# Kernel tuning notes

Measured on AMD Instinct MI355X. Metric: run time of the kernel, lower is better.

## Reference

```python
import jax, jax.numpy as jnp
import numpy as np

P = 512        # number of graph pairs
MAXN = 192     # max(len_s) by construction
D_IN = 32      # num_input_features
HID = 64       # hidden_dim
REG = 0.1      # entropic reg
ITERS = 8      # numItermax in forward call
DEG = 8        # avg degree for synthetic edges


def setup_inputs() -> dict:
    key = jax.random.key(0)
    ks = jax.random.split(key, 16)
    len_s = np.asarray(96 + (np.arange(P) % 97), dtype=np.int32)          # 96..192
    len_t = np.asarray(32 + ((np.arange(P) * 7) % 65), dtype=np.int32)    # 32..96 <= len_s
    Ns, Nt = int(len_s.sum()), int(len_t.sum())
    return {
        "x_s": jax.random.normal(ks[0], (Ns, D_IN), jnp.float32),
        "x_t": jax.random.normal(ks[1], (Nt, D_IN), jnp.float32),
        "W_rel0": 0.1 * jax.random.normal(ks[2], (D_IN, HID), jnp.float32),
        "b_rel0": 0.1 * jax.random.normal(ks[3], (HID,), jnp.float32),
        "W_root0": 0.1 * jax.random.normal(ks[4], (D_IN, HID), jnp.float32),
        "W_rel1": 0.1 * jax.random.normal(ks[5], (HID, HID), jnp.float32),
        "b_rel1": 0.1 * jax.random.normal(ks[6], (HID,), jnp.float32),
        "W_root1": 0.1 * jax.random.normal(ks[7], (HID, HID), jnp.float32),
        "W_e": 0.1 * jax.random.normal(ks[8], (D_IN + 2 * HID, 64), jnp.float32),
        "b_e": 0.1 * jax.random.normal(ks[9], (64,), jnp.float32),
        "virtual": jax.random.uniform(ks[10], (64,), jnp.float32),
        "edge_index_s": jax.random.randint(ks[11], (2, Ns * DEG), 0, Ns, dtype=jnp.int32),
        "edge_index_t": jax.random.randint(ks[12], (2, Nt * DEG), 0, Nt, dtype=jnp.int32),
        "len_s": jnp.asarray(len_s),
        "len_t": jnp.asarray(len_t),
    }


def _normalize(x):
    return x / jnp.clip(jnp.linalg.norm(x, axis=-1, keepdims=True), 1e-12)


def _gnn_embed(x, ei, layers, W_e, b_e):
    # GraphConv: out = lin_rel(sum_{j->i} x_j) + lin_root(x_i), then relu; cat all layer outputs
    outs = [x]
    h = x
    for (Wr, br, Wo) in layers:
        agg = jax.ops.segment_sum(h[ei[0]], ei[1], num_segments=h.shape[0])
        h = jax.nn.relu(agg @ Wr + br + h @ Wo)
        outs.append(h)
    emb = jnp.concatenate(outs, axis=1) @ W_e + b_e
    return _normalize(emb)


def _pad_gather(emb, lens):
    # [total, E] -> [P, MAXN, E] via per-pair offsets (indices clipped; invalid masked later)
    off = jnp.cumsum(lens) - lens
    idx = jnp.clip(off[:, None] + jnp.arange(MAXN)[None, :], 0, emb.shape[0] - 1)
    return emb[idx]


def reference(x_s, x_t, W_rel0, b_rel0, W_root0, W_rel1, b_rel1, W_root1,
              W_e, b_e, virtual, edge_index_s, edge_index_t, len_s, len_t):
    layers = [(W_rel0, b_rel0, W_root0), (W_rel1, b_rel1, W_root1)]
    emb_s = _gnn_embed(x_s, edge_index_s, layers, W_e, b_e)  # [Ns, 64]
    emb_t = _gnn_embed(x_t, edge_index_t, layers, W_e, b_e)  # [Nt, 64]
    virt = _normalize(virtual[None, :])[0]

    s_pad = _pad_gather(emb_s, len_s)  # [P, MAXN, 64]
    t_pad = _pad_gather(emb_t, len_t)  # [P, MAXN, 64]
    j = jnp.arange(MAXN)
    # columns >= len_t use the virtual node embedding (covers j in [m, n))
    t_mask = (j[None, :] < len_t[:, None])[:, :, None]
    t_aug = jnp.where(t_mask, t_pad, virt[None, None, :])

    # Euclidean cdist via quadratic expansion
    sq_s = jnp.sum(s_pad * s_pad, -1)                              # [P, MAXN]
    sq_t = jnp.sum(t_aug * t_aug, -1)                              # [P, MAXN]
    dot = jnp.einsum('pid,pjd->pij', s_pad, t_aug)                 # [P, MAXN, MAXN]
    cd = jnp.sqrt(jnp.maximum(sq_s[:, :, None] + sq_t[:, None, :] - 2.0 * dot, 1e-12))

    # padded cost: real block = cdist, bottom-right pad block = 0, rest = 1000
    row_valid = j[None, :] < len_s[:, None]                        # [P, MAXN] (n = len_s)
    in_block = row_valid[:, :, None] & row_valid[:, None, :]
    pad_block = (~row_valid)[:, :, None] & (~row_valid)[:, None, :]
    cost = jnp.where(in_block, cd, jnp.where(pad_block, 0.0, 1000.0))

    # Sinkhorn-Knopp, a = b = ones(MAXN) so Kp = K and updates are 1/(K v), 1/(K^T u)
    K = jnp.exp(-cost / REG)

    def body(_, uv):
        u, v = uv
        v = 1.0 / jnp.einsum('pij,pi->pj', K, u)
        u = 1.0 / jnp.einsum('pij,pj->pi', K, v)
        return (u, v)

    u0 = jnp.full((P, MAXN), 1.0 / MAXN, dtype=cost.dtype)
    u, v = jax.lax.fori_loop(0, ITERS, body, (u0, u0))
    gamma = jax.lax.stop_gradient(u[:, :, None] * K * v[:, None, :])

    geds = jnp.sum(gamma * cost, axis=(1, 2))
    geds2 = geds / (len_s + len_t).astype(cost.dtype)
    return gamma, cost, geds2
```

## Files before the change

### kernel.cpp

```cpp
#include <hip/hip_runtime.h>
#include <math.h>

#define PAIRS 512
#define MAXN 192

__global__ void offsets_kernel(const int* __restrict__ ls, const int* __restrict__ lt,
                               int* __restrict__ off) {
    __shared__ int wa[8], wb[8];
    int t = threadIdx.x;
    int a = ls[t], b = lt[t];
    int ia = a, ib = b;
#pragma unroll
    for (int d = 1; d < 64; d <<= 1) {
        int xa = __shfl_up(ia, d, 64);
        int xb = __shfl_up(ib, d, 64);
        if ((t & 63) >= d) { ia += xa; ib += xb; }
    }
    if ((t & 63) == 63) { wa[t >> 6] = ia; wb[t >> 6] = ib; }
    __syncthreads();
    int pa = 0, pb = 0;
    for (int w = 0; w < (t >> 6); w++) { pa += wa[w]; pb += wb[w]; }
    off[t] = pa + ia - a;
    off[PAIRS + t] = pb + ib - b;
}

__global__ __launch_bounds__(256) void count2_kernel(const int* __restrict__ eiS,
                                                     const int* __restrict__ eiT,
                                                     int* __restrict__ cnt,
                                                     int Es, int Et, int split) {
    int e = blockIdx.x * 256 + threadIdx.x;
    if (e < Es) atomicAdd(&cnt[eiS[Es + e]], 1);
    else if (e < Es + Et) atomicAdd(&cnt[split + eiT[Et + (e - Es)]], 1);
}

__global__ __launch_bounds__(256) void scan1_kernel(int* __restrict__ data,
                                                    int* __restrict__ blockSums, int N) {
    __shared__ int sc[256];
    int t = threadIdx.x;
    int base = blockIdx.x * 1024;
    int v[4];
    int s = 0;
#pragma unroll
    for (int q = 0; q < 4; q++) {
        int i = base + t * 4 + q;
        v[q] = (i < N) ? data[i] : 0;
        s += v[q];
    }
    sc[t] = s;
    __syncthreads();
    for (int d = 1; d < 256; d <<= 1) {
        int x = (t >= d) ? sc[t - d] : 0;
        __syncthreads();
        sc[t] += x;
        __syncthreads();
    }
    int excl = sc[t] - s;
#pragma unroll
    for (int q = 0; q < 4; q++) {
        int i = base + t * 4 + q;
        if (i < N) { data[i] = excl; excl += v[q]; }
    }
    if (t == 255) blockSums[blockIdx.x] = sc[255];
}

__global__ void scan2_kernel(int* __restrict__ blockSums, int B) {
    __shared__ int sh[256];
    int t = threadIdx.x;
    int v = (t < B) ? blockSums[t] : 0;
    sh[t] = v;
    __syncthreads();
    for (int d = 1; d < 256; d <<= 1) {
        int x = (t >= d) ? sh[t - d] : 0;
        __syncthreads();
        sh[t] += x;
        __syncthreads();
    }
    if (t < B) blockSums[t] = sh[t] - v;
}

__global__ __launch_bounds__(256) void scan3_kernel(int* __restrict__ data,
                                                    const int* __restrict__ blockSums,
                                                    int* __restrict__ cursor, int N) {
    int i = blockIdx.x * 256 + threadIdx.x;
    if (i < N) {
        int v = data[i] + blockSums[i >> 10];
        data[i] = v;
        cursor[i] = v;
    }
}

__global__ __launch_bounds__(256) void fill2_kernel(const int* __restrict__ eiS,
                                                    const int* __restrict__ eiT,
                                                    int* __restrict__ cursor,
                                                    int* __restrict__ src,
                                                    int Es, int Et, int split) {
    int e = blockIdx.x * 256 + threadIdx.x;
    if (e < Es) {
        int p = atomicAdd(&cursor[eiS[Es + e]], 1);
        src[p] = eiS[e];
    } else if (e < Es + Et) {
        int ee = e - Es;
        int p = atomicAdd(&cursor[split + eiT[Et + ee]], 1);
        src[p] = eiT[ee];
    }
}

template <int F>
__global__ __launch_bounds__(256) void gather_kernel(const float* __restrict__ featA,
                                                     const float* __restrict__ featB,
                                                     int split,
                                                     const int* __restrict__ rs,
                                                     const int* __restrict__ re,
                                                     const int* __restrict__ src,
                                                     float* __restrict__ agg, int N) {
    int gid = blockIdx.x * 256 + threadIdx.x;
    int row = gid / F;
    int lane = threadIdx.x & (F - 1);
    if (row >= N) return;
    int b = rs[row], e = re[row];
    int cnt = e - b;
    const float* feat = (row < split) ? featA : featB;
    int pre = cnt < F ? cnt : F;
    int sidx = (lane < cnt) ? src[b + lane] : 0;
    float acc = 0.f;
    for (int q = 0; q < pre; q++) {
        int s = __shfl(sidx, q, F);
        acc += feat[(size_t)s * F + lane];
    }
    for (int q = b + F; q < e; q++) acc += feat[(size_t)src[q] * F + lane];
    agg[(size_t)row * F + lane] = acc;
}

template <int KIN>
__global__ __launch_bounds__(256) void lin_gemm_kernel(const float* __restrict__ agg,
    const float* __restrict__ hinA, const float* __restrict__ hinB, int split,
    const float* __restrict__ Wrel, const float* __restrict__ brel,
    const float* __restrict__ Wroot, float* __restrict__ hout, int N) {
    __shared__ float Abuf[64 * 65];
    __shared__ float4 Wbuf[64 * 16];
    int tid = threadIdx.x;
    int i = tid & 15, j = tid >> 4;
    int rowbase = blockIdx.x * 64;
    float4 bv = ((const float4*)brel)[j];
    float acc[4][4];
#pragma unroll
    for (int r = 0; r < 4; r++) { acc[r][0] = bv.x; acc[r][1] = bv.y; acc[r][2] = bv.z; acc[r][3] = bv.w; }

    for (int c0 = 0; c0 < 2 * KIN; c0 += 64) {
        __syncthreads();
        for (int t = tid; t < 1024; t += 256) {
            int r = t >> 4, k4 = t & 15;
            int kg = c0 + 4 * k4;
            int row = rowbase + r; if (row >= N) row = N - 1;
            float4 v;
            if (kg < KIN) {
                v = ((const float4*)(agg + (size_t)row * KIN))[kg >> 2];
            } else {
                int kk = kg - KIN;
                const float* h = (row < split) ? hinA + (size_t)row * KIN
                                               : hinB + (size_t)(row - split) * KIN;
                v = ((const float4*)h)[kk >> 2];
            }
            float* d = Abuf + r * 65 + 4 * k4;
            d[0] = v.x; d[1] = v.y; d[2] = v.z; d[3] = v.w;
        }
        for (int t = tid; t < 1024; t += 256) {
            int k = t >> 4, jj = t & 15;
            int kg = c0 + k;
            const float* Wsrc = (kg < KIN) ? (Wrel + (size_t)kg * 64)
                                           : (Wroot + (size_t)(kg - KIN) * 64);
            Wbuf[t] = ((const float4*)Wsrc)[jj];
        }
        __syncthreads();
#pragma unroll 4
        for (int k = 0; k < 64; k++) {
            float4 wv = Wbuf[k * 16 + j];
            float a0 = Abuf[(4 * i + 0) * 65 + k];
            float a1 = Abuf[(4 * i + 1) * 65 + k];
            float a2 = Abuf[(4 * i + 2) * 65 + k];
            float a3 = Abuf[(4 * i + 3) * 65 + k];
            acc[0][0] = fmaf(a0, wv.x, acc[0][0]); acc[0][1] = fmaf(a0, wv.y, acc[0][1]);
            acc[0][2] = fmaf(a0, wv.z, acc[0][2]); acc[0][3] = fmaf(a0, wv.w, acc[0][3]);
            acc[1][0] = fmaf(a1, wv.x, acc[1][0]); acc[1][1] = fmaf(a1, wv.y, acc[1][1]);
            acc[1][2] = fmaf(a1, wv.z, acc[1][2]); acc[1][3] = fmaf(a1, wv.w, acc[1][3]);
            acc[2][0] = fmaf(a2, wv.x, acc[2][0]); acc[2][1] = fmaf(a2, wv.y, acc[2][1]);
            acc[2][2] = fmaf(a2, wv.z, acc[2][2]); acc[2][3] = fmaf(a2, wv.w, acc[2][3]);
            acc[3][0] = fmaf(a3, wv.x, acc[3][0]); acc[3][1] = fmaf(a3, wv.y, acc[3][1]);
            acc[3][2] = fmaf(a3, wv.z, acc[3][2]); acc[3][3] = fmaf(a3, wv.w, acc[3][3]);
        }
    }
#pragma unroll
    for (int r = 0; r < 4; r++) {
        int row = rowbase + 4 * i + r;
        if (row < N) {
            float4 o = make_float4(fmaxf(acc[r][0], 0.f), fmaxf(acc[r][1], 0.f),
                                   fmaxf(acc[r][2], 0.f), fmaxf(acc[r][3], 0.f));
            ((float4*)(hout + (size_t)row * 64))[j] = o;
        }
    }
}

__global__ __launch_bounds__(256) void emb_gemm_kernel(const float* __restrict__ xA,
    const float* __restrict__ xB, int split,
    const float* __restrict__ h1, const float* __restrict__ h2,
    const float* __restrict__ We, const float* __restrict__ be,
    float* __restrict__ emb, int N) {
    __shared__ float Abuf[64 * 65];
    __shared__ float4 Wbuf[64 * 16];
    int tid = threadIdx.x;
    int i = tid & 15, j = tid >> 4;
    int rowbase = blockIdx.x * 64;
    float4 bv = ((const float4*)be)[j];
    float acc[4][4];
#pragma unroll
    for (int r = 0; r < 4; r++) { acc[r][0] = bv.x; acc[r][1] = bv.y; acc[r][2] = bv.z; acc[r][3] = bv.w; }

    for (int c0 = 0; c0 < 160; c0 += 64) {
        int kw = (160 - c0 < 64) ? (160 - c0) : 64;
        int sh = (kw == 64) ? 4 : 3;
        int msk = (1 << sh) - 1;
        __syncthreads();
        for (int t = tid; t < 64 * (kw >> 2); t += 256) {
            int r = t >> sh, k4 = t & msk;
            int kg = c0 + 4 * k4;
            int row = rowbase + r; if (row >= N) row = N - 1;
            float4 v;
            if (kg < 32) {
                const float* x = (row < split) ? xA + (size_t)row * 32
                                               : xB + (size_t)(row - split) * 32;
                v = ((const float4*)x)[kg >> 2];
            } else if (kg < 96) {
                v = ((const float4*)(h1 + (size_t)row * 64))[(kg - 32) >> 2];
            } else {
                v = ((const float4*)(h2 + (size_t)row * 64))[(kg - 96) >> 2];
            }
            float* d = Abuf + r * 65 + 4 * k4;
            d[0] = v.x; d[1] = v.y; d[2] = v.z; d[3] = v.w;
        }
        for (int t = tid; t < kw * 16; t += 256) {
            int k = t >> 4, jj = t & 15;
            Wbuf[t] = ((const float4*)(We + (size_t)(c0 + k) * 64))[jj];
        }
        __syncthreads();
#pragma unroll 4
        for (int k = 0; k < kw; k++) {
            float4 wv = Wbuf[k * 16 + j];
            float a0 = Abuf[(4 * i + 0) * 65 + k];
            float a1 = Abuf[(4 * i + 1) * 65 + k];
            float a2 = Abuf[(4 * i + 2) * 65 + k];
            float a3 = Abuf[(4 * i + 3) * 65 + k];
            acc[0][0] = fmaf(a0, wv.x, acc[0][0]); acc[0][1] = fmaf(a0, wv.y, acc[0][1]);
            acc[0][2] = fmaf(a0, wv.z, acc[0][2]); acc[0][3] = fmaf(a0, wv.w, acc[0][3]);
            acc[1][0] = fmaf(a1, wv.x, acc[1][0]); acc[1][1] = fmaf(a1, wv.y, acc[1][1]);
            acc[1][2] = fmaf(a1, wv.z, acc[1][2]); acc[1][3] = fmaf(a1, wv.w, acc[1][3]);
            acc[2][0] = fmaf(a2, wv.x, acc[2][0]); acc[2][1] = fmaf(a2, wv.y, acc[2][1]);
            acc[2][2] = fmaf(a2, wv.z, acc[2][2]); acc[2][3] = fmaf(a2, wv.w, acc[2][3]);
            acc[3][0] = fmaf(a3, wv.x, acc[3][0]); acc[3][1] = fmaf(a3, wv.y, acc[3][1]);
            acc[3][2] = fmaf(a3, wv.z, acc[3][2]); acc[3][3] = fmaf(a3, wv.w, acc[3][3]);
        }
    }
    __syncthreads();
#pragma unroll
    for (int r = 0; r < 4; r++)
#pragma unroll
        for (int c = 0; c < 4; c++)
            Abuf[(4 * i + r) * 65 + 4 * j + c] = acc[r][c];
    __syncthreads();
    int lane = tid & 63, wv = tid >> 6;
    for (int rr = 0; rr < 16; rr++) {
        int r = wv * 16 + rr;
        float val = Abuf[r * 65 + lane];
        float ss = val * val;
#pragma unroll
        for (int d = 32; d > 0; d >>= 1) ss += __shfl_xor(ss, d, 64);
        int row = rowbase + r;
        if (row < N) emb[(size_t)row * 64 + lane] = val / fmaxf(sqrtf(ss), 1e-12f);
    }
}

__global__ __launch_bounds__(1024, 1) void cost_sink_kernel(const float* __restrict__ embS,
                                                            const float* __restrict__ embT,
                                                            const float* __restrict__ vraw,
                                                            const int* __restrict__ lenS,
                                                            const int* __restrict__ lenT,
                                                            const int* __restrict__ off,
                                                            float* __restrict__ cost,
                                                            float* __restrict__ gamma,
                                                            float* __restrict__ geds2,
                                                            int Ns) {
    __shared__ float sST[24960];
    __shared__ float part[32 * 193];
    __shared__ float u[MAXN];
    __shared__ float v[MAXN];
    __shared__ float sqS[MAXN];
    __shared__ float sqT[MAXN];
    __shared__ __align__(16) float virt[64];
    __shared__ float wsum[16];

    int p = blockIdx.x;
    int tid = threadIdx.x;
    int ti = tid & 31, tj = tid >> 5;
    int n = lenS[p], m = lenT[p];
    int offs = off[p], offt = off[PAIRS + p];
    float* sS = sST;
    float* sT = sST + 12480;

    if (tid < 64) {
        float vv = vraw[tid];
        float ss = vv * vv;
#pragma unroll
        for (int d = 32; d > 0; d >>= 1) ss += __shfl_xor(ss, d, 64);
        virt[tid] = vv / fmaxf(sqrtf(ss), 1e-12f);
    }
    __syncthreads();

    for (int t = tid; t < 192 * 16; t += 1024) {
        int r = t >> 4, q = t & 15;
        int gi = offs + r; if (gi > Ns - 1) gi = Ns - 1;
        float4 vv = ((const float4*)embS)[(size_t)gi * 16 + q];
        float* d = sS + r * 65 + q * 4;
        d[0] = vv.x; d[1] = vv.y; d[2] = vv.z; d[3] = vv.w;
    }
    for (int t = tid; t < 192 * 16; t += 1024) {
        int j = t >> 4, q = t & 15;
        float4 vv;
        if (j < m) vv = ((const float4*)embT)[(size_t)(offt + j) * 16 + q];
        else       vv = ((const float4*)virt)[q];
        float* d = sT + j * 65 + q * 4;
        d[0] = vv.x; d[1] = vv.y; d[2] = vv.z; d[3] = vv.w;
    }
    __syncthreads();

    if (tid < 192) {
        float s = 0.f;
#pragma unroll
        for (int k = 0; k < 64; k++) { float a = sS[tid * 65 + k]; s = fmaf(a, a, s); }
        sqS[tid] = s;
    } else if (tid < 384) {
        int j = tid - 192;
        float s = 0.f;
#pragma unroll
        for (int k = 0; k < 64; k++) { float a = sT[j * 65 + k]; s = fmaf(a, a, s); }
        sqT[j] = s;
    }
    __syncthreads();

    float kt[6][6];
#pragma unroll
    for (int r = 0; r < 6; r++)
#pragma unroll
        for (int c = 0; c < 6; c++) kt[r][c] = 0.f;

    int ib = ti * 6, jb = tj * 6;
    for (int k = 0; k < 64; k++) {
        float sv[6], tv[6];
#pragma unroll
        for (int r = 0; r < 6; r++) sv[r] = sS[(ib + r) * 65 + k];
#pragma unroll
        for (int c = 0; c < 6; c++) tv[c] = sT[(jb + c) * 65 + k];
#pragma unroll
        for (int r = 0; r < 6; r++)
#pragma unroll
            for (int c = 0; c < 6; c++) kt[r][c] = fmaf(sv[r], tv[c], kt[r][c]);
    }
#pragma unroll
    for (int r = 0; r < 6; r++) {
        int i = ib + r;
        bool rv = i < n;
        float sqi = sqS[i];
#pragma unroll
        for (int c = 0; c < 6; c++) {
            int j = jb + c;
            float cd = sqrtf(fmaxf(sqi + sqT[j] - 2.f * kt[r][c], 1e-12f));
            bool cv = j < n;
            kt[r][c] = (rv && cv) ? cd : ((!rv && !cv) ? 0.f : 1000.f);
        }
    }

    float* bounce = sST;
    float* cp = cost + (size_t)p * MAXN * MAXN;
    for (int h = 0; h < 2; h++) {
        __syncthreads();
        if ((ti >> 4) == h) {
            int rb = ib - 96 * h;
#pragma unroll
            for (int r = 0; r < 6; r++)
#pragma unroll
                for (int c = 0; c < 6; c++)
                    bounce[(rb + r) * 193 + jb + c] = kt[r][c];
        }
        __syncthreads();
        for (int q = 0; q < 18; q++) {
            int el = q * 1024 + tid;
            int row = el / 192, col = el - row * 192;
            cp[(size_t)(96 * h + row) * 192 + col] = bounce[row * 193 + col];
        }
    }

#pragma unroll
    for (int r = 0; r < 6; r++)
#pragma unroll
        for (int c = 0; c < 6; c++) kt[r][c] = expf(-10.f * kt[r][c]);

    if (tid < MAXN) u[tid] = 1.f / 192.f;

    for (int it = 0; it < 8; it++) {
        __syncthreads();
        {
            float ur[6];
#pragma unroll
            for (int r = 0; r < 6; r++) ur[r] = u[ib + r];
#pragma unroll
            for (int c = 0; c < 6; c++) {
                float s = 0.f;
#pragma unroll
                for (int r = 0; r < 6; r++) s = fmaf(kt[r][c], ur[r], s);
                part[ti * 193 + jb + c] = s;
            }
        }
        __syncthreads();
        if (tid < MAXN) {
            float s = 0.f;
#pragma unroll
            for (int q = 0; q < 32; q++) s += part[q * 193 + tid];
            v[tid] = 1.f / s;
        }
        __syncthreads();
        {
            float vc[6];
#pragma unroll
            for (int c = 0; c < 6; c++) vc[c] = v[jb + c];
#pragma unroll
            for (int r = 0; r < 6; r++) {
                float s = 0.f;
#pragma unroll
                for (int c = 0; c < 6; c++) s = fmaf(kt[r][c], vc[c], s);
                part[tj * 193 + ib + r] = s;
            }
        }
        __syncthreads();
        if (tid < MAXN) {
            float s = 0.f;
#pragma unroll
            for (int q = 0; q < 32; q++) s += part[q * 193 + tid];
            u[tid] = 1.f / s;
        }
    }
    __syncthreads();

    float ur[6], vc[6];
#pragma unroll
    for (int r = 0; r < 6; r++) ur[r] = u[ib + r];
#pragma unroll
    for (int c = 0; c < 6; c++) vc[c] = v[jb + c];

    float acc = 0.f;
#pragma unroll
    for (int r = 0; r < 6; r++)
#pragma unroll
        for (int c = 0; c < 6; c++) {
            float kk = kt[r][c];
            float g = ur[r] * kk * vc[c];
            if (kk > 0.f) acc = fmaf(g, -0.1f * logf(kk), acc);
        }
#pragma unroll
    for (int d = 32; d > 0; d >>= 1) acc += __shfl_xor(acc, d, 64);
    if ((tid & 63) == 0) wsum[tid >> 6] = acc;

    float* gp = gamma + (size_t)p * MAXN * MAXN;
    for (int h = 0; h < 2; h++) {
        __syncthreads();
        if ((ti >> 4) == h) {
            int rb = ib - 96 * h;
#pragma unroll
            for (int r = 0; r < 6; r++)
#pragma unroll
                for (int c = 0; c < 6; c++)
                    bounce[(rb + r) * 193 + jb + c] = ur[r] * kt[r][c] * vc[c];
        }
        __syncthreads();
        for (int q = 0; q < 18; q++) {
            int el = q * 1024 + tid;
            int row = el / 192, col = el - row * 192;
            gp[(size_t)(96 * h + row) * 192 + col] = bounce[row * 193 + col];
        }
    }
    if (tid == 0) {
        float s = 0.f;
        for (int q = 0; q < 16; q++) s += wsum[q];
        geds2[p] = s / (float)(n + m);
    }
}

extern "C" void kernel_launch(void* const* d_in, const int* in_sizes, int n_in,
                              void* d_out, int out_size, void* d_ws, size_t ws_size,
                              hipStream_t stream) {
    const float* x_s     = (const float*)d_in[0];
    const float* x_t     = (const float*)d_in[1];
    const float* W_rel0  = (const float*)d_in[2];
    const float* b_rel0  = (const float*)d_in[3];
    const float* W_root0 = (const float*)d_in[4];
    const float* W_rel1  = (const float*)d_in[5];
    const float* b_rel1  = (const float*)d_in[6];
    const float* W_root1 = (const float*)d_in[7];
    const float* W_e     = (const float*)d_in[8];
    const float* b_e     = (const float*)d_in[9];
    const float* virt    = (const float*)d_in[10];
    const int*   ei_s    = (const int*)d_in[11];
    const int*   ei_t    = (const int*)d_in[12];
    const int*   len_s   = (const int*)d_in[13];
    const int*   len_t   = (const int*)d_in[14];

    int Ns = in_sizes[0] / 32;
    int Nt = in_sizes[1] / 32;
    int Es = in_sizes[11] / 2;
    int Et = in_sizes[12] / 2;
    int Ntot = Ns + Nt;
    int Etot = Es + Et;

    char* w = (char*)d_ws;
    int* off  = (int*)w;              w += 1024 * 4;
    int* bsum = (int*)w;              w += 256 * 4;
    int* rs   = (int*)w;              w += (size_t)Ntot * 4;
    int* cur  = (int*)w;              w += (size_t)Ntot * 4;
    int* src  = (int*)w;              w += (size_t)Etot * 4;
    w = (char*)(((size_t)w + 255) & ~(size_t)255);
    float* agg = (float*)w;           w += (size_t)Ntot * 64 * 4;
    float* h1  = (float*)w;           w += (size_t)Ntot * 64 * 4;
    float* h2  = (float*)w;           w += (size_t)Ntot * 64 * 4;

    float* out_gamma = (float*)d_out;
    float* out_cost  = out_gamma + (size_t)PAIRS * MAXN * MAXN;
    float* out_geds  = out_cost + (size_t)PAIRS * MAXN * MAXN;

    offsets_kernel<<<1, PAIRS, 0, stream>>>(len_s, len_t, off);

    hipMemsetAsync(rs, 0, (size_t)Ntot * 4, stream);
    count2_kernel<<<(Etot + 255) / 256, 256, 0, stream>>>(ei_s, ei_t, rs, Es, Et, Ns);
    int nb = (Ntot + 1023) / 1024;
    scan1_kernel<<<nb, 256, 0, stream>>>(rs, bsum, Ntot);
    scan2_kernel<<<1, 256, 0, stream>>>(bsum, nb);
    scan3_kernel<<<(Ntot + 255) / 256, 256, 0, stream>>>(rs, bsum, cur, Ntot);
    fill2_kernel<<<(Etot + 255) / 256, 256, 0, stream>>>(ei_s, ei_t, cur, src, Es, Et, Ns);

    int gblk = (Ntot + 63) / 64;

    gather_kernel<32><<<(int)(((long long)Ntot * 32 + 255) / 256), 256, 0, stream>>>(
        x_s, x_t, Ns, rs, cur, src, agg, Ntot);
    lin_gemm_kernel<32><<<gblk, 256, 0, stream>>>(
        agg, x_s, x_t, Ns, W_rel0, b_rel0, W_root0, h1, Ntot);
    gather_kernel<64><<<(int)(((long long)Ntot * 64 + 255) / 256), 256, 0, stream>>>(
        h1, h1 + (size_t)Ns * 64, Ns, rs, cur, src, agg, Ntot);
    lin_gemm_kernel<64><<<gblk, 256, 0, stream>>>(
        agg, h1, h1, Ntot + 1, W_rel1, b_rel1, W_root1, h2, Ntot);
    emb_gemm_kernel<<<gblk, 256, 0, stream>>>(
        x_s, x_t, Ns, h1, h2, W_e, b_e, agg, Ntot);

    cost_sink_kernel<<<PAIRS, 1024, 0, stream>>>(
        agg, agg + (size_t)Ns * 64, virt, len_s, len_t, off,
        out_cost, out_gamma, out_geds, Ns);
}
```

Before: 651.1 us.

## Shrink LDS footprint and use shuffle reductions in cost/Sinkhorn kernel

Cuts LDS use by staging the embedding tiles in two 32-column chunks and replacing the 32-way partial-sum column reduction with wavefront xor-shuffles. This drops the v array and one barrier per Sinkhorn iteration. Squared norms are assumed to be 1 because embeddings are L2-normalized, which removes the norm pass but depends on that normalization holding. Cost and gamma writeback now goes in three 64-row slices through a padded bounce buffer with 16-byte nontemporal stores. The launch-bounds hint is raised so more than one block can fit per CU.

```diff
diff --git a/kernel.cpp b/kernel.cpp
--- a/kernel.cpp
+++ b/kernel.cpp
@@ -3,6 +3,8 @@
 
 #define PAIRS 512
 #define MAXN 192
+
+typedef float f4 __attribute__((ext_vector_type(4)));
 
 __global__ void offsets_kernel(const int* __restrict__ ls, const int* __restrict__ lt,
                                int* __restrict__ off) {
@@ -278,7 +280,7 @@
     }
 }
 
-__global__ __launch_bounds__(1024, 1) void cost_sink_kernel(const float* __restrict__ embS,
+__global__ __launch_bounds__(1024, 8) void cost_sink_kernel(const float* __restrict__ embS,
                                                             const float* __restrict__ embT,
                                                             const float* __restrict__ vraw,
                                                             const int* __restrict__ lenS,
@@ -288,22 +290,20 @@
                                                             float* __restrict__ gamma,
                                                             float* __restrict__ geds2,
                                                             int Ns) {
-    __shared__ float sST[24960];
-    __shared__ float part[32 * 193];
+    __shared__ __align__(16) float ldsST[12672];
+    __shared__ float part[16 * 200];
     __shared__ float u[MAXN];
-    __shared__ float v[MAXN];
-    __shared__ float sqS[MAXN];
-    __shared__ float sqT[MAXN];
     __shared__ __align__(16) float virt[64];
     __shared__ float wsum[16];
 
     int p = blockIdx.x;
     int tid = threadIdx.x;
     int ti = tid & 31, tj = tid >> 5;
+    int ib = ti * 6, jb = tj * 6;
     int n = lenS[p], m = lenT[p];
     int offs = off[p], offt = off[PAIRS + p];
-    float* sS = sST;
-    float* sT = sST + 12480;
+    float* stS = ldsST;
+    float* stT = ldsST + 6336;
 
     if (tid < 64) {
         float vv = vraw[tid];
@@ -312,38 +312,7 @@
         for (int d = 32; d > 0; d >>= 1) ss += __shfl_xor(ss, d, 64);
         virt[tid] = vv / fmaxf(sqrtf(ss), 1e-12f);
     }
-    __syncthreads();
-
-    for (int t = tid; t < 192 * 16; t += 1024) {
-        int r = t >> 4, q = t & 15;
-        int gi = offs + r; if (gi > Ns - 1) gi = Ns - 1;
-        float4 vv = ((const float4*)embS)[(size_t)gi * 16 + q];
-        float* d = sS + r * 65 + q * 4;
-        d[0] = vv.x; d[1] = vv.y; d[2] = vv.z; d[3] = vv.w;
-    }
-    for (int t = tid; t < 192 * 16; t += 1024) {
-        int j = t >> 4, q = t & 15;
-        float4 vv;
-        if (j < m) vv = ((const float4*)embT)[(size_t)(offt + j) * 16 + q];
-        else       vv = ((const float4*)virt)[q];
-        float* d = sT + j * 65 + q * 4;
-        d[0] = vv.x; d[1] = vv.y; d[2] = vv.z; d[3] = vv.w;
-    }
-    __syncthreads();
-
-    if (tid < 192) {
-        float s = 0.f;
-#pragma unroll
-        for (int k = 0; k < 64; k++) { float a = sS[tid * 65 + k]; s = fmaf(a, a, s); }
-        sqS[tid] = s;
-    } else if (tid < 384) {
-        int j = tid - 192;
-        float s = 0.f;
-#pragma unroll
-        for (int k = 0; k < 64; k++) { float a = sT[j * 65 + k]; s = fmaf(a, a, s); }
-        sqT[j] = s;
-    }
-    __syncthreads();
+    if (tid < MAXN) u[tid] = 1.f / 192.f;
 
     float kt[6][6];
 #pragma unroll
@@ -351,49 +320,69 @@
 #pragma unroll
         for (int c = 0; c < 6; c++) kt[r][c] = 0.f;
 
-    int ib = ti * 6, jb = tj * 6;
-    for (int k = 0; k < 64; k++) {
-        float sv[6], tv[6];
-#pragma unroll
-        for (int r = 0; r < 6; r++) sv[r] = sS[(ib + r) * 65 + k];
-#pragma unroll
-        for (int c = 0; c < 6; c++) tv[c] = sT[(jb + c) * 65 + k];
-#pragma unroll
-        for (int r = 0; r < 6; r++)
-#pragma unroll
-            for (int c = 0; c < 6; c++) kt[r][c] = fmaf(sv[r], tv[c], kt[r][c]);
-    }
+    for (int c0 = 0; c0 < 64; c0 += 32) {
+        __syncthreads();
+        int q0 = c0 >> 2;
+        for (int t = tid; t < 192 * 8; t += 1024) {
+            int r = t >> 3, q = t & 7;
+            int gi = offs + r; if (gi > Ns - 1) gi = Ns - 1;
+            float4 vv = ((const float4*)embS)[(size_t)gi * 16 + q0 + q];
+            float* d = stS + r * 33 + 4 * q;
+            d[0] = vv.x; d[1] = vv.y; d[2] = vv.z; d[3] = vv.w;
+        }
+        for (int t = tid; t < 192 * 8; t += 1024) {
+            int j = t >> 3, q = t & 7;
+            float4 vv;
+            if (j < m) vv = ((const float4*)embT)[(size_t)(offt + j) * 16 + q0 + q];
+            else       vv = ((const float4*)virt)[q0 + q];
+            float* d = stT + j * 33 + 4 * q;
+            d[0] = vv.x; d[1] = vv.y; d[2] = vv.z; d[3] = vv.w;
+        }
+        __syncthreads();
+        for (int k = 0; k < 32; k++) {
+            float sv[6], tv[6];
+#pragma unroll
+            for (int r = 0; r < 6; r++) sv[r] = stS[(ib + r) * 33 + k];
+#pragma unroll
+            for (int c = 0; c < 6; c++) tv[c] = stT[(jb + c) * 33 + k];
+#pragma unroll
+            for (int r = 0; r < 6; r++)
+#pragma unroll
+                for (int c = 0; c < 6; c++) kt[r][c] = fmaf(sv[r], tv[c], kt[r][c]);
+        }
+    }
+
 #pragma unroll
     for (int r = 0; r < 6; r++) {
         int i = ib + r;
         bool rv = i < n;
-        float sqi = sqS[i];
 #pragma unroll
         for (int c = 0; c < 6; c++) {
             int j = jb + c;
-            float cd = sqrtf(fmaxf(sqi + sqT[j] - 2.f * kt[r][c], 1e-12f));
+            float cd = sqrtf(fmaxf(2.f - 2.f * kt[r][c], 1e-12f));
             bool cv = j < n;
             kt[r][c] = (rv && cv) ? cd : ((!rv && !cv) ? 0.f : 1000.f);
         }
     }
 
-    float* bounce = sST;
+    float* bounce = ldsST;
     float* cp = cost + (size_t)p * MAXN * MAXN;
-    for (int h = 0; h < 2; h++) {
-        __syncthreads();
-        if ((ti >> 4) == h) {
-            int rb = ib - 96 * h;
-#pragma unroll
-            for (int r = 0; r < 6; r++)
-#pragma unroll
-                for (int c = 0; c < 6; c++)
-                    bounce[(rb + r) * 193 + jb + c] = kt[r][c];
-        }
-        __syncthreads();
-        for (int q = 0; q < 18; q++) {
-            int el = q * 1024 + tid;
-            int row = el / 192, col = el - row * 192;
-            cp[(size_t)(96 * h + row) * 192 + col] = bounce[row * 193 + col];
+    for (int sl = 0; sl < 3; sl++) {
+        __syncthreads();
+#pragma unroll
+        for (int r = 0; r < 6; r++) {
+            int row = ib + r;
+            if ((row >> 6) == sl) {
+                float* br = bounce + (row - (sl << 6)) * 196 + jb;
+#pragma unroll
+                for (int c = 0; c < 6; c++) br[c] = kt[r][c];
+            }
+        }
+        __syncthreads();
+        for (int t = tid; t < 3072; t += 1024) {
+            int row = t / 48, q4 = t - row * 48;
+            f4 vv = *(const f4*)(bounce + row * 196 + 4 * q4);
+            __builtin_nontemporal_store(vv, (f4*)(cp + (size_t)((sl << 6) + row) * 192 + 4 * q4));
         }
     }
 
@@ -402,58 +391,55 @@
 #pragma unroll
         for (int c = 0; c < 6; c++) kt[r][c] = expf(-10.f * kt[r][c]);
 
-    if (tid < MAXN) u[tid] = 1.f / 192.f;
-
+    float vc[6];
     for (int it = 0; it < 8; it++) {
         __syncthreads();
-        {
-            float ur[6];
-#pragma unroll
-            for (int r = 0; r < 6; r++) ur[r] = u[ib + r];
-#pragma unroll
-            for (int c = 0; c < 6; c++) {
-                float s = 0.f;
-#pragma unroll
-                for (int r = 0; r < 6; r++) s = fmaf(kt[r][c], ur[r], s);
-                part[ti * 193 + jb + c] = s;
-            }
+        float ur[6];
+#pragma unroll
+        for (int r = 0; r < 6; r++) ur[r] = u[ib + r];
+        float pc[6];
+#pragma unroll
+        for (int c = 0; c < 6; c++) {
+            float s = 0.f;
+#pragma unroll
+            for (int r = 0; r < 6; r++) s = fmaf(kt[r][c], ur[r], s);
+            pc[c] = s;
+        }
+#pragma unroll
+        for (int mask = 1; mask <= 16; mask <<= 1)
+#pragma unroll
+            for (int c = 0; c < 6; c++) pc[c] += __shfl_xor(pc[c], mask, 64);
+#pragma unroll
+        for (int c = 0; c < 6; c++) vc[c] = 1.f / pc[c];
+
+        float pr[6];
+#pragma unroll
+        for (int r = 0; r < 6; r++) {
+            float s = 0.f;
+#pragma unroll
+            for (int c = 0; c < 6; c++) s = fmaf(kt[r][c], vc[c], s);
+            pr[r] = s;
+        }
+#pragma unroll
+        for (int r = 0; r < 6; r++) pr[r] += __shfl_xor(pr[r], 32, 64);
+        if ((tid & 63) < 32) {
+            int w = tid >> 6;
+#pragma unroll
+            for (int r = 0; r < 6; r++) part[w * 200 + ib + r] = pr[r];
         }
         __syncthreads();
         if (tid < MAXN) {
             float s = 0.f;
 #pragma unroll
-            for (int q = 0; q < 32; q++) s += part[q * 193 + tid];
-            v[tid] = 1.f / s;
-        }
-        __syncthreads();
-        {
-            float vc[6];
-#pragma unroll
-            for (int c = 0; c < 6; c++) vc[c] = v[jb + c];
-#pragma unroll
-            for (int r = 0; r < 6; r++) {
-                float s = 0.f;
-#pragma unroll
-                for (int c = 0; c < 6; c++) s = fmaf(kt[r][c], vc[c], s);
-                part[tj * 193 + ib + r] = s;
-            }
-        }
-        __syncthreads();
-        if (tid < MAXN) {
-            float s = 0.f;
-#pragma unroll
-            for (int q = 0; q < 32; q++) s += part[q * 193 + tid];
+            for (int w = 0; w < 16; w++) s += part[w * 200 + tid];
             u[tid] = 1.f / s;
         }
     }
     __syncthreads();
 
-    float ur[6], vc[6];
+    float ur[6];
 #pragma unroll
     for (int r = 0; r < 6; r++) ur[r] = u[ib + r];
-#pragma unroll
-    for (int c = 0; c < 6; c++) vc[c] = v[jb + c];
-
     float acc = 0.f;
 #pragma unroll
     for (int r = 0; r < 6; r++)
@@ -468,21 +454,22 @@
     if ((tid & 63) == 0) wsum[tid >> 6] = acc;
 
     float* gp = gamma + (size_t)p * MAXN * MAXN;
-    for (int h = 0; h < 2; h++) {
-        __syncthreads();
-        if ((ti >> 4) == h) {
-            int rb = ib - 96 * h;
-#pragma unroll
-            for (int r = 0; r < 6; r++)
-#pragma unroll
-                for (int c = 0; c < 6; c++)
-                    bounce[(rb + r) * 193 + jb + c] = ur[r] * kt[r][c] * vc[c];
-        }
-        __syncthreads();
-        for (int q = 0; q < 18; q++) {
-            int el = q * 1024 + tid;
-            int row = el / 192, col = el - row * 192;
-            gp[(size_t)(96 * h + row) * 192 + col] = bounce[row * 193 + col];
+    for (int sl = 0; sl < 3; sl++) {
+        __syncthreads();
+#pragma unroll
+        for (int r = 0; r < 6; r++) {
+            int row = ib + r;
+            if ((row >> 6) == sl) {
+                float* br = bounce + (row - (sl << 6)) * 196 + jb;
+#pragma unroll
+                for (int c = 0; c < 6; c++) br[c] = ur[r] * kt[r][c] * vc[c];
+            }
+        }
+        __syncthreads();
+        for (int t = tid; t < 3072; t += 1024) {
+            int row = t / 48, q4 = t - row * 48;
+            f4 vv = *(const f4*)(bounce + row * 196 + 4 * q4);
+            __builtin_nontemporal_store(vv, (f4*)(gp + (size_t)((sl << 6) + row) * 192 + 4 * q4));
         }
     }
     if (tid == 0) {
@@ -535,7 +522,7 @@
 
     offsets_kernel<<<1, PAIRS, 0, stream>>>(len_s, len_t, off);
 
-    hipMemsetAsync(rs, 0, (size_t)Ntot * 4, stream);
+    (void)hipMemsetAsync(rs, 0, (size_t)Ntot * 4, stream);
     count2_kernel<<<(Etot + 255) / 256, 256, 0, stream>>>(ei_s, ei_t, rs, Es, Et, Ns);
     int nb = (Ntot + 1023) / 1024;
     scan1_kernel<<<nb, 256, 0, stream>>>(rs, bsum, Ntot);
```

After: 1.448 ms. +122.4%, slower.
